# Kernel tuning notes

Hardware: AMD Instinct MI355X
Metric: run time of the kernel (lower is better)

## Reference

```python
import jax, jax.numpy as jnp
import numpy as np

N = 10000
E = 160000
IN_CH = 128
HID = 128
HEADS = 4
OUT_CH = 1  # forced by nn.Linear(heads, 1) applied after conv2


def _linear_params(key, out_f, in_f):
    k1, k2 = jax.random.split(key)
    bound = 1.0 / np.sqrt(in_f)
    W = jax.random.uniform(k1, (out_f, in_f), jnp.float32, -bound, bound)
    b = jax.random.uniform(k2, (out_f,), jnp.float32, -bound, bound)
    return W, b


def setup_inputs() -> dict:
    key = jax.random.key(0)
    ks = jax.random.split(key, 12)
    x = jax.random.normal(ks[0], (N, IN_CH), jnp.float32)
    edge_index = jax.random.randint(ks[1], (2, E), 0, N, jnp.int64)

    # conv1: TransformerConv(IN_CH, HID, HEADS)
    Wq1, bq1 = _linear_params(ks[2], HEADS * HID, IN_CH)
    Wk1, bk1 = _linear_params(ks[3], HEADS * HID, IN_CH)
    Wv1, bv1 = _linear_params(ks[4], HEADS * HID, IN_CH)
    Ws1, bs1 = _linear_params(ks[5], HEADS * HID, IN_CH)  # root/skip

    # conv2: TransformerConv(HID*HEADS, OUT_CH, HEADS)
    d2 = HID * HEADS
    Wq2, bq2 = _linear_params(ks[6], HEADS * OUT_CH, d2)
    Wk2, bk2 = _linear_params(ks[7], HEADS * OUT_CH, d2)
    Wv2, bv2 = _linear_params(ks[8], HEADS * OUT_CH, d2)
    Ws2, bs2 = _linear_params(ks[9], HEADS * OUT_CH, d2)

    # final nn.Linear(HEADS, 1)
    Wl, bl = _linear_params(ks[10], 1, HEADS)

    return dict(x=x, edge_index=edge_index,
                Wq1=Wq1, bq1=bq1, Wk1=Wk1, bk1=bk1, Wv1=Wv1, bv1=bv1, Ws1=Ws1, bs1=bs1,
                Wq2=Wq2, bq2=bq2, Wk2=Wk2, bk2=bk2, Wv2=Wv2, bv2=bv2, Ws2=Ws2, bs2=bs2,
                Wl=Wl, bl=bl)


def transformer_conv(x, edge_index, Wq, bq, Wk, bk, Wv, bv, Ws, bs, heads, ch):
    # PyG TransformerConv defaults: concat=True, root_weight=True, beta=False
    n = x.shape[0]
    q = (x @ Wq.T + bq).reshape(n, heads, ch)
    k = (x @ Wk.T + bk).reshape(n, heads, ch)
    v = (x @ Wv.T + bv).reshape(n, heads, ch)

    src, dst = edge_index[0], edge_index[1]  # messages flow src -> dst
    # per-edge attention logits [E, H]
    logits = jnp.einsum('ehc,ehc->eh', q[dst], k[src]) / np.sqrt(ch).astype(np.float32)

    # segment softmax over edges grouped by destination node
    seg_max = jax.ops.segment_max(logits, dst, num_segments=n)  # [N, H]
    seg_max = jnp.where(jnp.isfinite(seg_max), seg_max, 0.0)
    ex = jnp.exp(logits - seg_max[dst])
    denom = jax.ops.segment_sum(ex, dst, num_segments=n)  # [N, H]
    alpha = ex / jnp.maximum(denom[dst], 1e-16)  # [E, H]

    # scatter-aggregate weighted values
    msgs = alpha[:, :, None] * v[src]  # [E, H, C]
    out = jax.ops.segment_sum(msgs, dst, num_segments=n)  # [N, H, C]
    out = out.reshape(n, heads * ch)
    # root/skip connection
    return out + (x @ Ws.T + bs)


def reference(x, edge_index,
              Wq1, bq1, Wk1, bk1, Wv1, bv1, Ws1, bs1,
              Wq2, bq2, Wk2, bk2, Wv2, bv2, Ws2, bs2,
              Wl, bl):
    h = transformer_conv(x, edge_index, Wq1, bq1, Wk1, bk1, Wv1, bv1, Ws1, bs1, HEADS, HID)
    h = jax.nn.relu(h)
    # dropout is identity in eval mode
    h = transformer_conv(h, edge_index, Wq2, bq2, Wk2, bk2, Wv2, bv2, Ws2, bs2, HEADS, OUT_CH)
    h = h @ Wl.T + bl  # [N, 1]
    return jnp.mean(h, axis=0, keepdims=True)  # [1, 1]
```

## Files before the change

kernel.cpp:

```cpp
#include <hip/hip_runtime.h>
#include <math.h>

#define NN 10000
#define NE 160000
#define NROWT 79
#define NGEMM (NROWT * 32)

typedef __attribute__((ext_vector_type(8))) short bf16x8;
typedef __attribute__((ext_vector_type(4))) float f32x4;
typedef __attribute__((ext_vector_type(2))) float f32x2;

#if defined(__has_builtin)
#if __has_builtin(__builtin_amdgcn_cvt_pk_fp8_f32) && __has_builtin(__builtin_amdgcn_cvt_pk_f32_fp8)
#define HW_FP8 1
#endif
#endif

__device__ inline ushort f2bf(float x) {
  uint u = __float_as_uint(x);
  return (ushort)((u + 0x7fffu + ((u >> 16) & 1u)) >> 16);
}

__device__ inline void unpack8(uint4 u, float* f) {
  f[0] = __uint_as_float(u.x << 16); f[1] = __uint_as_float(u.x & 0xffff0000u);
  f[2] = __uint_as_float(u.y << 16); f[3] = __uint_as_float(u.y & 0xffff0000u);
  f[4] = __uint_as_float(u.z << 16); f[5] = __uint_as_float(u.z & 0xffff0000u);
  f[6] = __uint_as_float(u.w << 16); f[7] = __uint_as_float(u.w & 0xffff0000u);
}

#ifndef HW_FP8
__device__ inline float fp8_dec1(uint b) {
  uint s = b >> 7, e = (b >> 3) & 15, m = b & 7;
  float v = (e == 0) ? ldexpf((float)m, -9) : ldexpf((float)(8 + m), (int)e - 10);
  return s ? -v : v;
}
__device__ inline uint fp8_enc1(float x) {
  uint s = (__float_as_uint(x) >> 31) << 7;
  float a = fabsf(x);
  if (!(a < 448.f)) return s | 0x7e;
  if (a < 9.765625e-4f) return s;
  int e; float m = frexpf(a, &e);
  int E = e - 1, q;
  if (E < -6) {
    q = (int)rintf(ldexpf(a, 9));
    if (q == 0) return s;
    if (q >= 8) return s | 8;
    return s | (uint)q;
  }
  q = (int)rintf(ldexpf(m, 4));
  if (q == 16) { q = 8; ++E; }
  if (E > 8 || (E == 8 && q == 15)) return s | 0x7e;
  return s | ((uint)(E + 7) << 3) | (uint)(q - 8);
}
#endif

__device__ inline uint pack4_fp8(float a, float b, float c, float d) {
#ifdef HW_FP8
  uint w = (uint)__builtin_amdgcn_cvt_pk_fp8_f32(a, b, 0, false);
  w = (uint)__builtin_amdgcn_cvt_pk_fp8_f32(c, d, (int)w, true);
  return w;
#else
  return fp8_enc1(a) | (fp8_enc1(b) << 8) | (fp8_enc1(c) << 16) | (fp8_enc1(d) << 24);
#endif
}

__device__ inline void dec8_fp8(uint lo, uint hi, float* f) {
#ifdef HW_FP8
  f32x2 p0 = __builtin_amdgcn_cvt_pk_f32_fp8((int)lo, false);
  f32x2 p1 = __builtin_amdgcn_cvt_pk_f32_fp8((int)lo, true);
  f32x2 p2 = __builtin_amdgcn_cvt_pk_f32_fp8((int)hi, false);
  f32x2 p3 = __builtin_amdgcn_cvt_pk_f32_fp8((int)hi, true);
  f[0] = p0.x; f[1] = p0.y; f[2] = p1.x; f[3] = p1.y;
  f[4] = p2.x; f[5] = p2.y; f[6] = p3.x; f[7] = p3.y;
#else
  f[0] = fp8_dec1(lo & 255); f[1] = fp8_dec1((lo >> 8) & 255);
  f[2] = fp8_dec1((lo >> 16) & 255); f[3] = fp8_dec1(lo >> 24);
  f[4] = fp8_dec1(hi & 255); f[5] = fp8_dec1((hi >> 8) & 255);
  f[6] = fp8_dec1((hi >> 16) & 255); f[7] = fp8_dec1(hi >> 24);
#endif
}

__device__ inline void dec16(uint4 u, float* f) {
  dec8_fp8(u.x, u.y, f);
  dec8_fp8(u.z, u.w, f + 8);
}

__global__ __launch_bounds__(1024) void zero_k(
    int* __restrict__ deg, float* __restrict__ out)
{
  int i = blockIdx.x * 1024 + threadIdx.x;
  if (i < NN) deg[i] = 0;
  if (i == 0) out[0] = 0.f;
}

__global__ __launch_bounds__(256) void prep_k(
    const float* __restrict__ x,
    const float* __restrict__ Wq1, const float* __restrict__ Wk1,
    const float* __restrict__ Wv1, const float* __restrict__ Ws1,
    ushort* __restrict__ x_bf, ushort* __restrict__ w1bf,
    const int* __restrict__ dst, int* __restrict__ deg)
{
  int i = blockIdx.x * 256 + threadIdx.x;
  if (i < NE) atomicAdd(&deg[dst[i]], 1);
  const int n4x = NN * 32;
  const int n4w = 512 * 128 / 4;
  if (i < n4x) {
    float4 v = ((const float4*)x)[i];
    ushort4 o;
    o.x = f2bf(v.x); o.y = f2bf(v.y); o.z = f2bf(v.z); o.w = f2bf(v.w);
    ((ushort4*)x_bf)[i] = o;
  } else {
    int c = i - n4x;
    if (c < 4 * n4w) {
      int seg = c >> 14, k = c & 16383;
      const float* W = (seg == 0) ? Wq1 : (seg == 1) ? Wk1
                     : (seg == 2) ? Wv1 : Ws1;
      float4 v = ((const float4*)W)[k];
      ushort4 o;
      o.x = f2bf(v.x); o.y = f2bf(v.y); o.z = f2bf(v.z); o.w = f2bf(v.w);
      ((ushort4*)(w1bf + ((size_t)seg << 16)))[k] = o;
    }
  }
}

__global__ __launch_bounds__(1024) void scan_k(
    const int* __restrict__ deg, int* __restrict__ rowptr,
    int* __restrict__ cursor)
{
  __shared__ int wsum[16];
  int tid = threadIdx.x;
  int base = tid * 10;
  int loc[10]; int s = 0;
  #pragma unroll
  for (int i = 0; i < 10; ++i) {
    int v = (base + i < NN) ? deg[base + i] : 0;
    loc[i] = s; s += v;
  }
  int mysum = s;
  #pragma unroll
  for (int d = 1; d < 64; d <<= 1) {
    int v = __shfl_up(s, d);
    if ((tid & 63) >= d) s += v;
  }
  if ((tid & 63) == 63) wsum[tid >> 6] = s;
  __syncthreads();
  int woff = 0;
  for (int w = 0; w < (tid >> 6); ++w) woff += wsum[w];
  int excl = woff + s - mysum;
  #pragma unroll
  for (int i = 0; i < 10; ++i) {
    int idx = base + i;
    if (idx < NN) { int r = excl + loc[i]; rowptr[idx] = r; cursor[idx] = r; }
  }
  if (tid == 1023) rowptr[NN] = woff + s;
}

__global__ __launch_bounds__(256) void gemm_scatter(
    const ushort* __restrict__ xbf, const ushort* __restrict__ wbf,
    const float* __restrict__ bq, const float* __restrict__ bk,
    const float* __restrict__ bv, const float* __restrict__ bs,
    unsigned char* __restrict__ q8, unsigned char* __restrict__ kv8,
    ushort* __restrict__ h1b,
    const int* __restrict__ src, const int* __restrict__ dst,
    int* __restrict__ cursor, int* __restrict__ csr_src)
{
  if (blockIdx.x >= NGEMM) {
    int e = (blockIdx.x - NGEMM) * 256 + threadIdx.x;
    if (e < NE) {
      int pos = atomicAdd(&cursor[dst[e]], 1);
      csr_src[pos] = src[e];
    }
    return;
  }
  __shared__ __align__(16) ushort Al[128 * 128];
  __shared__ __align__(16) ushort Bl[64 * 128];
  const int row0 = (blockIdx.x % NROWT) << 7;
  const int ncol0 = (blockIdx.x / NROWT) << 6;
  const int tid = threadIdx.x;

  #pragma unroll
  for (int i = 0; i < 8; ++i) {
    int slot = tid + (i << 8);
    int r = slot >> 4, c = slot & 15;
    int gr = row0 + r;
    uint4 v = make_uint4(0u, 0u, 0u, 0u);
    if (gr < NN) v = *(const uint4*)(xbf + (size_t)gr * 128 + (c << 3));
    *(uint4*)(Al + r * 128 + ((c ^ (r & 7)) << 3)) = v;
  }
  #pragma unroll
  for (int i = 0; i < 4; ++i) {
    int slot = tid + (i << 8);
    int r = slot >> 4, c = slot & 15;
    uint4 v = *(const uint4*)(wbf + (size_t)(ncol0 + r) * 128 + (c << 3));
    *(uint4*)(Bl + r * 128 + ((c ^ (r & 7)) << 3)) = v;
  }
  __syncthreads();

  const int wid = tid >> 6, lane = tid & 63;
  const int wm = wid >> 1, wn = wid & 1;
  const int lr = lane & 15, lkg = lane >> 4;
  const int seg = ncol0 >> 9;
  const int colInSeg = ncol0 & 511;
  const bool swp = (seg < 3);

  f32x4 acc[4][2];
  #pragma unroll
  for (int m = 0; m < 4; ++m)
    #pragma unroll
    for (int n = 0; n < 2; ++n) acc[m][n] = (f32x4){0.f, 0.f, 0.f, 0.f};

  #pragma unroll
  for (int ks = 0; ks < 4; ++ks) {
    int c16 = (ks << 2) + lkg;
    bf16x8 a[4], b[2];
    #pragma unroll
    for (int mf = 0; mf < 4; ++mf) {
      int r = (wm << 6) + (mf << 4) + lr;
      a[mf] = *(const bf16x8*)(Al + r * 128 + ((c16 ^ (r & 7)) << 3));
    }
    #pragma unroll
    for (int nf = 0; nf < 2; ++nf) {
      int r = (wn << 5) + (nf << 4) + lr;
      b[nf] = *(const bf16x8*)(Bl + r * 128 + ((c16 ^ (r & 7)) << 3));
    }
    if (swp) {
      #pragma unroll
      for (int mf = 0; mf < 4; ++mf)
        #pragma unroll
        for (int nf = 0; nf < 2; ++nf)
          acc[mf][nf] = __builtin_amdgcn_mfma_f32_16x16x32_bf16(
              b[nf], a[mf], acc[mf][nf], 0, 0, 0);
    } else {
      #pragma unroll
      for (int mf = 0; mf < 4; ++mf)
        #pragma unroll
        for (int nf = 0; nf < 2; ++nf)
          acc[mf][nf] = __builtin_amdgcn_mfma_f32_16x16x32_bf16(
              a[mf], b[nf], acc[mf][nf], 0, 0, 0);
    }
  }

  const float* bias = (seg == 0) ? bq : (seg == 1) ? bk : (seg == 2) ? bv : bs;
  if (swp) {
    unsigned char* out8 = (seg == 0) ? q8 : kv8;
    const int rs = (seg == 0) ? 512 : 1024;
    const int choff = (seg == 2) ? 512 : 0;
    const float scale = (seg == 0) ? 0.08838834764831845f : 1.f;
    #pragma unroll
    for (int mf = 0; mf < 4; ++mf) {
      int xrow = row0 + (wm << 6) + (mf << 4) + lr;
      if (xrow >= NN) continue;
      #pragma unroll
      for (int nf = 0; nf < 2; ++nf) {
        int ch = colInSeg + (wn << 5) + (nf << 4) + (lkg << 2);
        float4 bb = *(const float4*)(bias + ch);
        uint w = pack4_fp8((acc[mf][nf][0] + bb.x) * scale,
                           (acc[mf][nf][1] + bb.y) * scale,
                           (acc[mf][nf][2] + bb.z) * scale,
                           (acc[mf][nf][3] + bb.w) * scale);
        *(uint*)(out8 + (size_t)xrow * rs + choff + ch) = w;
      }
    }
  } else {
    #pragma unroll
    for (int mf = 0; mf < 4; ++mf) {
      #pragma unroll
      for (int nf = 0; nf < 2; ++nf) {
        int col = colInSeg + (wn << 5) + (nf << 4) + lr;
        float bb = bias[col];
        #pragma unroll
        for (int r = 0; r < 4; ++r) {
          int row = row0 + (wm << 6) + (mf << 4) + (lkg << 2) + r;
          if (row >= NN) continue;
          h1b[(size_t)row * 512 + col] = f2bf(acc[mf][nf][r] + bb);
        }
      }
    }
  }
}

#define EDGE_A(kvreg)                                                      \
  {                                                                        \
    float f[16]; dec16(kvreg, f);                                          \
    float t = qf[0]*f[0]+qf[1]*f[1]+qf[2]*f[2]+qf[3]*f[3]                  \
            + qf[4]*f[4]+qf[5]*f[5]+qf[6]*f[6]+qf[7]*f[7]                  \
            + qf[8]*f[8]+qf[9]*f[9]+qf[10]*f[10]+qf[11]*f[11]              \
            + qf[12]*f[12]+qf[13]*f[13]+qf[14]*f[14]+qf[15]*f[15];         \
    t += __shfl_xor(t, 1);                                                 \
    t += __shfl_xor(t, 2);                                                 \
    t += __shfl_xor(t, 4);                                                 \
    float exA = __expf(t);                                                 \
    float exO = __shfl_xor(exA, 32);                                       \
    if (kl) den += exA;                                                    \
    float exV = kl ? 0.f : exO;                                            \
    _Pragma("unroll")                                                      \
    for (int i = 0; i < 16; ++i) acc[i] = fmaf(exV, f[i], acc[i]);         \
  }

__global__ __launch_bounds__(256) void attn1(
    const unsigned char* __restrict__ q8, const unsigned char* __restrict__ kv8,
    const int* __restrict__ rowptr, const int* __restrict__ csr_src,
    ushort* __restrict__ h1b)
{
  const int n = blockIdx.x * 4 + (threadIdx.x >> 6);
  const int lane = threadIdx.x & 63;
  const bool kl = lane < 32;
  const int vl = lane & 31;

  float qf[16];
  if (kl) {
    uint4 qv = *(const uint4*)(q8 + (size_t)n * 512 + (lane << 4));
    dec16(qv, qf);
  } else {
    #pragma unroll
    for (int i = 0; i < 16; ++i) qf[i] = 0.f;
  }

  float acc[16] = {};
  float den = 0.f;
  int j = rowptr[n];
  const int e1 = rowptr[n + 1];
  for (; j + 3 < e1; j += 4) {
    int s0 = csr_src[j], s1 = csr_src[j + 1];
    int s2 = csr_src[j + 2], s3 = csr_src[j + 3];
    uint4 a0 = *(const uint4*)(kv8 + (size_t)s0 * 1024 + (lane << 4));
    uint4 a1 = *(const uint4*)(kv8 + (size_t)s1 * 1024 + (lane << 4));
    uint4 a2 = *(const uint4*)(kv8 + (size_t)s2 * 1024 + (lane << 4));
    uint4 a3 = *(const uint4*)(kv8 + (size_t)s3 * 1024 + (lane << 4));
    EDGE_A(a0)
    EDGE_A(a1)
    EDGE_A(a2)
    EDGE_A(a3)
  }
  for (; j < e1; ++j) {
    int s0 = csr_src[j];
    uint4 a0 = *(const uint4*)(kv8 + (size_t)s0 * 1024 + (lane << 4));
    EDGE_A(a0)
  }

  float dAll = kl ? den : 0.f;
  float dv = __shfl_xor(dAll, 32);
  if (!kl) {
    float inv = 1.f / fmaxf(dv, 1e-16f);
    int c0 = vl << 4;
    float sk[16];
    uint4 s0 = *(const uint4*)(h1b + (size_t)n * 512 + c0);
    uint4 s1 = *(const uint4*)(h1b + (size_t)n * 512 + c0 + 8);
    unpack8(s0, sk); unpack8(s1, sk + 8);
    ushort o[16];
    #pragma unroll
    for (int i = 0; i < 16; ++i)
      o[i] = f2bf(fmaxf(sk[i] + acc[i] * inv, 0.f));
    uint4 w0, w1;
    w0.x = (uint)o[0]  | ((uint)o[1]  << 16);
    w0.y = (uint)o[2]  | ((uint)o[3]  << 16);
    w0.z = (uint)o[4]  | ((uint)o[5]  << 16);
    w0.w = (uint)o[6]  | ((uint)o[7]  << 16);
    w1.x = (uint)o[8]  | ((uint)o[9]  << 16);
    w1.y = (uint)o[10] | ((uint)o[11] << 16);
    w1.z = (uint)o[12] | ((uint)o[13] << 16);
    w1.w = (uint)o[14] | ((uint)o[15] << 16);
    *(uint4*)(h1b + (size_t)n * 512 + c0) = w0;
    *(uint4*)(h1b + (size_t)n * 512 + c0 + 8) = w1;
  }
}

__global__ __launch_bounds__(256) void gemm_l2(
    const ushort* __restrict__ h1b,
    const float* __restrict__ Wq, const float* __restrict__ bq,
    const float* __restrict__ Wk, const float* __restrict__ bk,
    const float* __restrict__ Wv, const float* __restrict__ bv,
    const float* __restrict__ Ws, const float* __restrict__ bs,
    float* __restrict__ qkv2, float* __restrict__ acc2)
{
  __shared__ float red[4][64][17];
  int n0 = blockIdx.x * 64;
  int wid = threadIdx.x >> 6, lane = threadIdx.x & 63;
  int n = n0 + lane;
  const float* Wm[4] = {Wq, Wk, Wv, Ws};
  float s[16] = {};
  if (n < NN) {
    const ushort* a = h1b + (size_t)n * 512 + wid * 128;
    #pragma unroll 2
    for (int i = 0; i < 128; i += 8) {
      uint4 hv = *(const uint4*)(a + i);
      float av[8]; unpack8(hv, av);
      #pragma unroll
      for (int j = 0; j < 16; ++j) {
        const float* w = Wm[j >> 2] + (size_t)(j & 3) * 512 + wid * 128 + i;
        s[j] += av[0]*w[0] + av[1]*w[1] + av[2]*w[2] + av[3]*w[3]
              + av[4]*w[4] + av[5]*w[5] + av[6]*w[6] + av[7]*w[7];
      }
    }
  }
  #pragma unroll
  for (int j = 0; j < 16; ++j) red[wid][lane][j] = s[j];
  __syncthreads();
  #pragma unroll
  for (int q = 0; q < 4; ++q) {
    int idx = threadIdx.x * 4 + q;
    int ln = idx >> 4, j = idx & 15;
    int nn2 = n0 + ln;
    if (nn2 >= NN) continue;
    float v = red[0][ln][j] + red[1][ln][j] + red[2][ln][j] + red[3][ln][j];
    int sg = j >> 2, r = j & 3;
    const float* bb = (sg == 0) ? bq : (sg == 1) ? bk : (sg == 2) ? bv : bs;
    v += bb[r];
    if (sg < 3) qkv2[nn2 * 12 + sg * 4 + r] = v;
    else        acc2[nn2 * 4 + r] = v;
  }
}

__global__ __launch_bounds__(256) void attn2_final(
    const float* __restrict__ qkv2, const int* __restrict__ rowptr,
    const int* __restrict__ csr_src, const float* __restrict__ acc2,
    const float* __restrict__ Wl, const float* __restrict__ bl,
    float* __restrict__ out)
{
  __shared__ float red[4];
  int t = blockIdx.x * 256 + threadIdx.x;
  int n = t >> 4, h = (t >> 2) & 3, part = t & 3;
  float q = qkv2[n * 12 + h];
  float den = 0.f, acc = 0.f;
  int e1 = rowptr[n + 1];
  for (int j = rowptr[n] + part; j < e1; j += 4) {
    int s = csr_src[j];
    float k = qkv2[s * 12 + 4 + h];
    float v = qkv2[s * 12 + 8 + h];
    float ex = __expf(q * k);
    den += ex; acc += ex * v;
  }
  den += __shfl_xor(den, 1); acc += __shfl_xor(acc, 1);
  den += __shfl_xor(den, 2); acc += __shfl_xor(acc, 2);
  float c = 0.f;
  if (part == 0)
    c = (acc2[n * 4 + h] + acc / fmaxf(den, 1e-16f)) * Wl[h] * (1.0f / NN);
  if (t == 0) c += bl[0];
  c += __shfl_xor(c, 4);
  c += __shfl_xor(c, 8);
  c += __shfl_xor(c, 16);
  c += __shfl_xor(c, 32);
  if ((threadIdx.x & 63) == 0) red[threadIdx.x >> 6] = c;
  __syncthreads();
  if (threadIdx.x == 0)
    unsafeAtomicAdd(out, red[0] + red[1] + red[2] + red[3]);
}

extern "C" void kernel_launch(void* const* d_in, const int* in_sizes, int n_in,
                              void* d_out, int out_size, void* d_ws, size_t ws_size,
                              hipStream_t stream)
{
  const float* x   = (const float*)d_in[0];
  const int*   ei  = (const int*)d_in[1];
  const float *Wq1 = (const float*)d_in[2],  *bq1 = (const float*)d_in[3];
  const float *Wk1 = (const float*)d_in[4],  *bk1 = (const float*)d_in[5];
  const float *Wv1 = (const float*)d_in[6],  *bv1 = (const float*)d_in[7];
  const float *Ws1 = (const float*)d_in[8],  *bs1 = (const float*)d_in[9];
  const float *Wq2 = (const float*)d_in[10], *bq2 = (const float*)d_in[11];
  const float *Wk2 = (const float*)d_in[12], *bk2 = (const float*)d_in[13];
  const float *Wv2 = (const float*)d_in[14], *bv2 = (const float*)d_in[15];
  const float *Ws2 = (const float*)d_in[16], *bs2 = (const float*)d_in[17];
  const float *Wl  = (const float*)d_in[18], *bl  = (const float*)d_in[19];
  const int* srcp = ei;
  const int* dstp = ei + NE;

  unsigned char* q8  = (unsigned char*)d_ws;
  unsigned char* kv8 = q8 + (size_t)NN * 512;
  ushort* x_bf = (ushort*)(kv8 + (size_t)NN * 1024);
  ushort* w1bf = x_bf + (size_t)NN * 128;
  ushort* h1b  = w1bf + (size_t)2048 * 128;
  float*  qkv2 = (float*)(h1b + (size_t)NN * 512);
  float*  acc2 = qkv2 + (size_t)NN * 12;
  int*   deg     = (int*)(acc2 + (size_t)NN * 4);
  int*   rowptr  = deg + NN;
  int*   cursor  = rowptr + NN + 1;
  int*   csr_src = cursor + NN;

  zero_k<<<10, 1024, 0, stream>>>(deg, (float*)d_out);
  {
    const int total = NN * 32 + 4 * (512 * 128 / 4);
    prep_k<<<(total + 255) / 256, 256, 0, stream>>>(
        x, Wq1, Wk1, Wv1, Ws1, x_bf, w1bf, dstp, deg);
  }
  scan_k<<<1, 1024, 0, stream>>>(deg, rowptr, cursor);

  gemm_scatter<<<NGEMM + (NE + 255) / 256, 256, 0, stream>>>(
      x_bf, w1bf, bq1, bk1, bv1, bs1, q8, kv8, h1b,
      srcp, dstp, cursor, csr_src);

  attn1<<<NN / 4, 256, 0, stream>>>(q8, kv8, rowptr, csr_src, h1b);

  gemm_l2<<<(NN + 63) / 64, 256, 0, stream>>>(
      h1b, Wq2, bq2, Wk2, bk2, Wv2, bv2, Ws2, bs2, qkv2, acc2);

  attn2_final<<<NN * 16 / 256, 256, 0, stream>>>(
      qkv2, rowptr, csr_src, acc2, Wl, bl, (float*)d_out);
}
```

Before: 136.7 us.

## Fuse degree count and scan into conversion kernel; stage GEMM epilogue through LDS

Replaces the zero, prep and scan kernels with one launch. An extra block builds the destination-degree histogram in shared memory using LDS atomics and scans it, while the other blocks convert x and the weights to bf16. This removes two launches and the global atomics on deg. The GEMM epilogue now writes accumulators to an LDS tile and then emits 16-byte coalesced fp8/bf16 stores instead of scattered 4-byte and 2-byte stores. The cost is that a single block handles all 160K edges serially for the histogram, which may sit on the critical path, and the epilogue gains extra barriers.

```diff
diff --git a/kernel.cpp b/kernel.cpp
--- a/kernel.cpp
+++ b/kernel.cpp
@@ -5,6 +5,7 @@
 #define NE 160000
 #define NROWT 79
 #define NGEMM (NROWT * 32)
+#define NCONV 1506
 
 typedef __attribute__((ext_vector_type(8))) short bf16x8;
 typedef __attribute__((ext_vector_type(4))) float f32x4;
@@ -19,6 +20,9 @@
 __device__ inline ushort f2bf(float x) {
   uint u = __float_as_uint(x);
   return (ushort)((u + 0x7fffu + ((u >> 16) & 1u)) >> 16);
+}
+__device__ inline uint pk2bf(float a, float b) {
+  return (uint)f2bf(a) | ((uint)f2bf(b) << 16);
 }
 
 __device__ inline void unpack8(uint4 u, float* f) {
@@ -85,33 +89,24 @@
   dec8_fp8(u.z, u.w, f + 8);
 }
 
-__global__ __launch_bounds__(1024) void zero_k(
-    int* __restrict__ deg, float* __restrict__ out)
-{
-  int i = blockIdx.x * 1024 + threadIdx.x;
-  if (i < NN) deg[i] = 0;
-  if (i == 0) out[0] = 0.f;
-}
-
-__global__ __launch_bounds__(256) void prep_k(
+__global__ __launch_bounds__(256) void prep_csr(
     const float* __restrict__ x,
     const float* __restrict__ Wq1, const float* __restrict__ Wk1,
     const float* __restrict__ Wv1, const float* __restrict__ Ws1,
     ushort* __restrict__ x_bf, ushort* __restrict__ w1bf,
-    const int* __restrict__ dst, int* __restrict__ deg)
+    const int* __restrict__ dst, int* __restrict__ rowptr,
+    int* __restrict__ cursor, float* __restrict__ out)
 {
-  int i = blockIdx.x * 256 + threadIdx.x;
-  if (i < NE) atomicAdd(&deg[dst[i]], 1);
-  const int n4x = NN * 32;
-  const int n4w = 512 * 128 / 4;
-  if (i < n4x) {
-    float4 v = ((const float4*)x)[i];
-    ushort4 o;
-    o.x = f2bf(v.x); o.y = f2bf(v.y); o.z = f2bf(v.z); o.w = f2bf(v.w);
-    ((ushort4*)x_bf)[i] = o;
-  } else {
-    int c = i - n4x;
-    if (c < 4 * n4w) {
+  if (blockIdx.x < NCONV) {
+    int i = blockIdx.x * 256 + threadIdx.x;
+    const int n4x = NN * 32;
+    if (i < n4x) {
+      float4 v = ((const float4*)x)[i];
+      ushort4 o;
+      o.x = f2bf(v.x); o.y = f2bf(v.y); o.z = f2bf(v.z); o.w = f2bf(v.w);
+      ((ushort4*)x_bf)[i] = o;
+    } else {
+      int c = i - n4x;
       int seg = c >> 14, k = c & 16383;
       const float* W = (seg == 0) ? Wq1 : (seg == 1) ? Wk1
                      : (seg == 2) ? Wv1 : Ws1;
@@ -120,39 +115,43 @@
       o.x = f2bf(v.x); o.y = f2bf(v.y); o.z = f2bf(v.z); o.w = f2bf(v.w);
       ((ushort4*)(w1bf + ((size_t)seg << 16)))[k] = o;
     }
-  }
-}
-
-__global__ __launch_bounds__(1024) void scan_k(
-    const int* __restrict__ deg, int* __restrict__ rowptr,
-    int* __restrict__ cursor)
-{
-  __shared__ int wsum[16];
-  int tid = threadIdx.x;
-  int base = tid * 10;
-  int loc[10]; int s = 0;
-  #pragma unroll
-  for (int i = 0; i < 10; ++i) {
-    int v = (base + i < NN) ? deg[base + i] : 0;
-    loc[i] = s; s += v;
-  }
-  int mysum = s;
+    return;
+  }
+  __shared__ int hist[NN];
+  __shared__ int wpart[4];
+  const int tid = threadIdx.x;
+  for (int i = tid; i < NN; i += 256) hist[i] = 0;
+  if (tid == 0) out[0] = 0.f;
+  __syncthreads();
+  for (int e = tid; e < NE; e += 256) atomicAdd(&hist[dst[e]], 1);
+  __syncthreads();
+  const int base = tid * 40;
+  int s = 0;
+  for (int i = 0; i < 40; ++i) {
+    int idx = base + i;
+    if (idx < NN) s += hist[idx];
+  }
+  int lane = tid & 63, wv = tid >> 6;
+  int incl = s;
   #pragma unroll
   for (int d = 1; d < 64; d <<= 1) {
-    int v = __shfl_up(s, d);
-    if ((tid & 63) >= d) s += v;
-  }
-  if ((tid & 63) == 63) wsum[tid >> 6] = s;
+    int v = __shfl_up(incl, d);
+    if (lane >= d) incl += v;
+  }
+  if (lane == 63) wpart[wv] = incl;
   __syncthreads();
   int woff = 0;
-  for (int w = 0; w < (tid >> 6); ++w) woff += wsum[w];
-  int excl = woff + s - mysum;
-  #pragma unroll
-  for (int i = 0; i < 10; ++i) {
+  for (int w = 0; w < wv; ++w) woff += wpart[w];
+  int run = woff + incl - s;
+  for (int i = 0; i < 40; ++i) {
     int idx = base + i;
-    if (idx < NN) { int r = excl + loc[i]; rowptr[idx] = r; cursor[idx] = r; }
-  }
-  if (tid == 1023) rowptr[NN] = woff + s;
+    if (idx < NN) {
+      int h = hist[idx];
+      rowptr[idx] = run; cursor[idx] = run;
+      run += h;
+    }
+  }
+  if (tid == 255) rowptr[NN] = woff + incl;
 }
 
 __global__ __launch_bounds__(256) void gemm_scatter(
@@ -172,8 +171,9 @@
     }
     return;
   }
-  __shared__ __align__(16) ushort Al[128 * 128];
-  __shared__ __align__(16) ushort Bl[64 * 128];
+  __shared__ __align__(16) ushort LDSbuf[24576];
+  ushort* Al = LDSbuf;
+  ushort* Bl = LDSbuf + 16384;
   const int row0 = (blockIdx.x % NROWT) << 7;
   const int ncol0 = (blockIdx.x / NROWT) << 6;
   const int tid = threadIdx.x;
@@ -240,25 +240,42 @@
     }
   }
 
+  __syncthreads();
+  float* S = (float*)LDSbuf;
   const float* bias = (seg == 0) ? bq : (seg == 1) ? bk : (seg == 2) ? bv : bs;
+
   if (swp) {
+    const float scale = (seg == 0) ? 0.08838834764831845f : 1.f;
+    #pragma unroll
+    for (int mf = 0; mf < 4; ++mf) {
+      int rl = (wm << 6) + (mf << 4) + lr;
+      #pragma unroll
+      for (int nf = 0; nf < 2; ++nf) {
+        int cl = (wn << 5) + (nf << 4) + (lkg << 2);
+        float4 bb = *(const float4*)(bias + colInSeg + cl);
+        float4 o;
+        o.x = (acc[mf][nf][0] + bb.x) * scale;
+        o.y = (acc[mf][nf][1] + bb.y) * scale;
+        o.z = (acc[mf][nf][2] + bb.z) * scale;
+        o.w = (acc[mf][nf][3] + bb.w) * scale;
+        *(float4*)(S + rl * 68 + cl) = o;
+      }
+    }
+    __syncthreads();
     unsigned char* out8 = (seg == 0) ? q8 : kv8;
     const int rs = (seg == 0) ? 512 : 1024;
-    const int choff = (seg == 2) ? 512 : 0;
-    const float scale = (seg == 0) ? 0.08838834764831845f : 1.f;
-    #pragma unroll
-    for (int mf = 0; mf < 4; ++mf) {
-      int xrow = row0 + (wm << 6) + (mf << 4) + lr;
-      if (xrow >= NN) continue;
-      #pragma unroll
-      for (int nf = 0; nf < 2; ++nf) {
-        int ch = colInSeg + (wn << 5) + (nf << 4) + (lkg << 2);
-        float4 bb = *(const float4*)(bias + ch);
-        uint w = pack4_fp8((acc[mf][nf][0] + bb.x) * scale,
-                           (acc[mf][nf][1] + bb.y) * scale,
-                           (acc[mf][nf][2] + bb.z) * scale,
-                           (acc[mf][nf][3] + bb.w) * scale);
-        *(uint*)(out8 + (size_t)xrow * rs + choff + ch) = w;
+    const int choff = ((seg == 2) ? 512 : 0) + colInSeg;
+    for (int tt = tid; tt < 512; tt += 256) {
+      int row = tt >> 2, q4 = (tt & 3) << 4;
+      int grow = row0 + row;
+      if (grow < NN) {
+        const float* p = S + row * 68 + q4;
+        uint4 w;
+        w.x = pack4_fp8(p[0],  p[1],  p[2],  p[3]);
+        w.y = pack4_fp8(p[4],  p[5],  p[6],  p[7]);
+        w.z = pack4_fp8(p[8],  p[9],  p[10], p[11]);
+        w.w = pack4_fp8(p[12], p[13], p[14], p[15]);
+        *(uint4*)(out8 + (size_t)grow * rs + choff + q4) = w;
       }
     }
   } else {
@@ -266,13 +283,30 @@
     for (int mf = 0; mf < 4; ++mf) {
       #pragma unroll
       for (int nf = 0; nf < 2; ++nf) {
-        int col = colInSeg + (wn << 5) + (nf << 4) + lr;
-        float bb = bias[col];
+        int cl = (wn << 5) + (nf << 4) + lr;
+        float bb = bias[colInSeg + cl];
         #pragma unroll
         for (int r = 0; r < 4; ++r) {
-          int row = row0 + (wm << 6) + (mf << 4) + (lkg << 2) + r;
-          if (row >= NN) continue;
-          h1b[(size_t)row * 512 + col] = f2bf(acc[mf][nf][r] + bb);
+          int rl = (wm << 6) + (mf << 4) + (lkg << 2) + r;
+          S[rl * 68 + cl] = acc[mf][nf][r] + bb;
+        }
+      }
+    }
+    __syncthreads();
+    {
+      int tt = tid;
+      int row = tt >> 1, hf = (tt & 1) << 5;
+      int grow = row0 + row;
+      if (grow < NN) {
+        const float* p = S + row * 68 + hf;
+        #pragma unroll
+        for (int g = 0; g < 4; ++g) {
+          uint4 w;
+          w.x = pk2bf(p[g*8+0], p[g*8+1]);
+          w.y = pk2bf(p[g*8+2], p[g*8+3]);
+          w.z = pk2bf(p[g*8+4], p[g*8+5]);
+          w.w = pk2bf(p[g*8+6], p[g*8+7]);
+          *(uint4*)(h1b + (size_t)grow * 512 + colInSeg + hf + g * 8) = w;
         }
       }
     }
@@ -471,18 +505,13 @@
   ushort* h1b  = w1bf + (size_t)2048 * 128;
   float*  qkv2 = (float*)(h1b + (size_t)NN * 512);
   float*  acc2 = qkv2 + (size_t)NN * 12;
-  int*   deg     = (int*)(acc2 + (size_t)NN * 4);
-  int*   rowptr  = deg + NN;
+  int*   rowptr  = (int*)(acc2 + (size_t)NN * 4);
   int*   cursor  = rowptr + NN + 1;
   int*   csr_src = cursor + NN;
 
-  zero_k<<<10, 1024, 0, stream>>>(deg, (float*)d_out);
-  {
-    const int total = NN * 32 + 4 * (512 * 128 / 4);
-    prep_k<<<(total + 255) / 256, 256, 0, stream>>>(
-        x, Wq1, Wk1, Wv1, Ws1, x_bf, w1bf, dstp, deg);
-  }
-  scan_k<<<1, 1024, 0, stream>>>(deg, rowptr, cursor);
+  prep_csr<<<NCONV + 1, 256, 0, stream>>>(
+      x, Wq1, Wk1, Wv1, Ws1, x_bf, w1bf, dstp, rowptr, cursor,
+      (float*)d_out);
 
   gemm_scatter<<<NGEMM + (NE + 255) / 256, 256, 0, stream>>>(
       x_bf, w1bf, bq1, bk1, bv1, bs1, q8, kv8, h1b,
```

After: 266.3 us. 1.95x slower.
